# Performance work log

Hardware: AMD Instinct MI355X
Metric: run time of the kernel (lower is better)

Reference implementation:

```python
import jax, jax.numpy as jnp
import numpy as np

NUM_PATCHES = 16
FILTER_SIZE = 4
IN_CHANNELS = 64
OUT_CHANNELS = 256
BATCH = 64


def setup_inputs() -> dict:
    key = jax.random.key(0)
    k1, k2 = jax.random.split(key)
    D = NUM_PATCHES * FILTER_SIZE
    x = jax.random.normal(k1, (BATCH, IN_CHANNELS, D, D), dtype=jnp.float32)
    w = jax.random.normal(
        k2,
        (OUT_CHANNELS, IN_CHANNELS, NUM_PATCHES, NUM_PATCHES, FILTER_SIZE ** 2),
        dtype=jnp.float32,
    )
    return {"x": x, "w": w}


def reference(x, w):
    # x: (N, C, D, D) with D = P*f ; w: (O, C, P, P, f^2)
    N, C, D, _ = x.shape
    O, _, P, _, f2 = w.shape
    f = int(round(f2 ** 0.5))
    # non-overlapping unfold: (N,C,P,f,P,f) -> (N,C,P,P,f,f) -> (N,C,P,P,f^2)
    patches = x.reshape(N, C, P, f, P, f).transpose(0, 1, 2, 4, 3, 5).reshape(N, C, P, P, f2)
    # locally-connected contraction over in_channels and filter elements
    y = jnp.einsum('ncpqf,ocpqf->nopq', patches, w)
    scale = 1.0 / jnp.sqrt(jnp.asarray(f2 * C, dtype=x.dtype))
    return jax.nn.relu(y * scale)
```

## Files before the change

### kernel.cpp

```cpp
#include <hip/hip_runtime.h>


typedef short bf16x8 __attribute__((ext_vector_type(8)));
typedef short bf16x4 __attribute__((ext_vector_type(4)));
typedef float f32x4  __attribute__((ext_vector_type(4)));

__device__ __forceinline__ short f2bf(float f) {
    union { float f; unsigned u; } v; v.f = f;
    return (short)((v.u + 0x7FFFu + ((v.u >> 16) & 1u)) >> 16);
}

__device__ __forceinline__ bf16x8 pack8(f32x4 a, f32x4 b) {
    bf16x8 r;
    r[0] = f2bf(a[0]); r[1] = f2bf(a[1]); r[2] = f2bf(a[2]); r[3] = f2bf(a[3]);
    r[4] = f2bf(b[0]); r[5] = f2bf(b[1]); r[6] = f2bf(b[2]); r[7] = f2bf(b[3]);
    return r;
}

__device__ __forceinline__ void gload16(const void* g, void* l) {
    __builtin_amdgcn_global_load_lds(
        (const __attribute__((address_space(1))) void*)g,
        (__attribute__((address_space(3))) void*)l, 16, 0, 0);
}

__global__ __launch_bounds__(256)
void prep_unfold(const float* __restrict__ x, short* __restrict__ xT) {
    __shared__ __align__(16) char tile[16 * 2056];
    const int bid = blockIdx.x;
    const int p = bid >> 6, c = bid & 63;
    const int t = (int)threadIdx.x;

#pragma unroll
    for (int it = 0; it < 16; ++it) {
        const int id = it * 256 + t;
        const int n = id >> 6, fr = (id >> 4) & 3, cq = id & 15;
        const f32x4 v = *(const f32x4*)(x + (size_t)n * 262144u
                                          + (size_t)c * 4096u
                                          + (size_t)(4 * p + fr) * 64u
                                          + (size_t)(cq * 4));
        bf16x4 b; b[0] = f2bf(v[0]); b[1] = f2bf(v[1]);
                  b[2] = f2bf(v[2]); b[3] = f2bf(v[3]);
        *(bf16x4*)(tile + cq * 2056 + (fr >> 1) * 1024 + n * 16
                        + (fr & 1) * 8) = b;
    }
    __syncthreads();

#pragma unroll
    for (int it = 0; it < 8; ++it) {
        const int id = it * 256 + t;
        const int q = id >> 7, s = id & 127;
        const int koct = s >> 6, n = s & 63;
        const bf16x8 v = *(const bf16x8*)(tile + q * 2056 + koct * 1024 + n * 16);
        *(bf16x8*)(xT + (size_t)(p * 16 + q) * 65536u + (size_t)c * 1024u
                      + (size_t)koct * 512u + (size_t)n * 8u) = v;
    }
}

__global__ __launch_bounds__(512)
void locblock_gemm(const short* __restrict__ xT, const float* __restrict__ w,
                   float* __restrict__ ws2) {
    __shared__ __align__(16) char smem[3][41472];

    const int hw = blockIdx.x;
    const int lb = (hw & 7) * 32 + (hw >> 3);
    const int p  = lb >> 4;
    const int q2 = (lb >> 1) & 7;
    const int oh = lb & 1;

    const int tid  = (int)threadIdx.x;
    const int lane = tid & 63;
    const int wv   = tid >> 6;
    const int l15  = lane & 15;
    const int kq   = lane >> 4;
    const int qw   = wv & 1;
    const int nc   = wv >> 1;

    const int qin  = wv >> 2, acf = (wv >> 1) & 1, akoct = wv & 1;
    const short* asrc = xT + (size_t)(p * 16 + q2 * 2 + qin) * 65536u
                           + (size_t)acf * 1024u + (size_t)akoct * 512u
                           + (size_t)lane * 8u;

    const float* wsrc[4];
#pragma unroll
    for (int j = 0; j < 4; ++j) {
        const int id = j * 512 + tid;
        const int ol = id >> 4, s = id & 15;
        const int u = s ^ (ol & 15);
        wsrc[j] = w + (size_t)(oh * 128 + ol) * 262144u + (size_t)(u >> 3) * 4096u
                    + (size_t)p * 256u + (size_t)(q2 * 32) + (size_t)((u & 7) * 4);
    }

    int aoff[4], boff[2][2];
#pragma unroll
    for (int mf = 0; mf < 4; ++mf)
        aoff[mf] = (qw * 4 + kq) * 1088 + (mf * 16 + l15) * 16;
    {
        const int u1 = (kq >> 1) * 8 + qw * 4 + (kq & 1) * 2;
#pragma unroll
        for (int nf = 0; nf < 2; ++nf) {
            const int ol = nc * 32 + nf * 16 + l15;
            boff[nf][0] = 8704 + ol * 256 + ((u1       ^ l15) * 16);
            boff[nf][1] = 8704 + ol * 256 + (((u1 + 1) ^ l15) * 16);
        }
    }

    f32x4 acc[4][2];
#pragma unroll
    for (int mf = 0; mf < 4; ++mf)
#pragma unroll
        for (int nf = 0; nf < 2; ++nf)
            acc[mf][nf] = (f32x4){0.f, 0.f, 0.f, 0.f};

    auto stage = [&](int t, int buf) {
        char* base = smem[buf];
        gload16(asrc + (size_t)t * 2048u, base + wv * 1088);
#pragma unroll
        for (int j = 0; j < 4; ++j)
            gload16(wsrc[j] + (size_t)t * 8192u,
                    base + 8704 + j * 8192 + wv * 1024);
    };

    auto compute = [&](int buf) {
        const char* Lb = smem[buf];
        bf16x8 av[4], bv[2];
#pragma unroll
        for (int mf = 0; mf < 4; ++mf)
            av[mf] = *(const bf16x8*)(Lb + aoff[mf]);
#pragma unroll
        for (int nf = 0; nf < 2; ++nf)
            bv[nf] = pack8(*(const f32x4*)(Lb + boff[nf][0]),
                           *(const f32x4*)(Lb + boff[nf][1]));
#pragma unroll
        for (int mf = 0; mf < 4; ++mf)
#pragma unroll
            for (int nf = 0; nf < 2; ++nf)
                acc[mf][nf] = __builtin_amdgcn_mfma_f32_16x16x32_bf16(
                    av[mf], bv[nf], acc[mf][nf], 0, 0, 0);
    };

    stage(0, 0);
    stage(1, 1);
    stage(2, 2);
#pragma unroll 1
    for (int t = 0; t < 29; ++t) {
        const int buf = t % 3;
        asm volatile("s_waitcnt vmcnt(10)" ::: "memory");
        __builtin_amdgcn_s_barrier();
        compute(buf);
        asm volatile("s_waitcnt lgkmcnt(0)" ::: "memory");
        __builtin_amdgcn_s_barrier();
        stage(t + 3, buf);
    }
    asm volatile("s_waitcnt vmcnt(10)" ::: "memory");
    __builtin_amdgcn_s_barrier();
    compute(2);
    asm volatile("s_waitcnt vmcnt(5)" ::: "memory");
    __builtin_amdgcn_s_barrier();
    compute(0);
    asm volatile("s_waitcnt vmcnt(0)" ::: "memory");
    __builtin_amdgcn_s_barrier();
    compute(1);

    const float scale = 0.03125f;
    const int pq = p * 16 + q2 * 2 + qw;
#pragma unroll
    for (int mf = 0; mf < 4; ++mf)
#pragma unroll
        for (int nf = 0; nf < 2; ++nf) {
            const int o  = oh * 128 + nc * 32 + nf * 16 + l15;
            const int n0 = mf * 16 + kq * 4;
            f32x4 r;
#pragma unroll
            for (int j = 0; j < 4; ++j)
                r[j] = fmaxf(acc[mf][nf][j] * scale, 0.0f);
            *(f32x4*)(ws2 + (size_t)pq * 16384u + (size_t)o * 64u + n0) = r;
        }
}

__global__ __launch_bounds__(256)
void finish_transpose(const float* __restrict__ ws2, float* __restrict__ out) {
    __shared__ float tile[256 * 68];
    const int o = blockIdx.x;
    const int t = (int)threadIdx.x;

#pragma unroll
    for (int it = 0; it < 16; ++it) {
        const int chunk = it * 256 + t;
        const int pq = chunk >> 4, ng = chunk & 15;
        const f32x4 v = *(const f32x4*)(ws2 + (size_t)pq * 16384u
                                            + (size_t)o * 64u + ng * 4);
        *(f32x4*)&tile[pq * 68 + ng * 4] = v;
    }
    __syncthreads();

    const int n = t >> 2, pqq = t & 3;
#pragma unroll
    for (int i = 0; i < 16; ++i) {
        const int pq0 = i * 16 + pqq * 4;
        f32x4 r;
#pragma unroll
        for (int k = 0; k < 4; ++k)
            r[k] = tile[(pq0 + k) * 68 + n];
        *(f32x4*)(out + (size_t)n * 65536u + (size_t)o * 256u + pq0) = r;
    }
}

extern "C" void kernel_launch(void* const* d_in, const int* in_sizes, int n_in,
                              void* d_out, int out_size, void* d_ws, size_t ws_size,
                              hipStream_t stream) {
    const float* x = (const float*)d_in[0];
    const float* w = (const float*)d_in[1];
    float* out = (float*)d_out;
    short* xT  = (short*)d_ws;
    float* ws2 = (float*)((char*)d_ws + (33554432));
    prep_unfold     <<<dim3(1024), dim3(256), 0, stream>>>(x, xT);
    locblock_gemm   <<<dim3(256),  dim3(512), 0, stream>>>(xT, w, ws2);
    finish_transpose<<<dim3(256),  dim3(256), 0, stream>>>(ws2, out);
}
```

Measured before the change: 104.8 us.

## Replace LDS-direct triple buffering with register-staged double-buffered pipeline

The GEMM kernel no longer uses global_load_lds into a three-stage LDS ring. A operands (bf16 activations) are now loaded straight into registers for each wave's own fragments. Weight tiles are loaded into registers and then written to a two-buffer swizzled LDS area. This cuts LDS footprint and allows the A path to bypass LDS, but it adds register pressure, explicit ds_writes, and a shallower prefetch distance. The hand-placed vmcnt waits must match the new load counts.

```diff
diff --git a/kernel.cpp b/kernel.cpp
--- a/kernel.cpp
+++ b/kernel.cpp
@@ -15,12 +15,6 @@
     r[0] = f2bf(a[0]); r[1] = f2bf(a[1]); r[2] = f2bf(a[2]); r[3] = f2bf(a[3]);
     r[4] = f2bf(b[0]); r[5] = f2bf(b[1]); r[6] = f2bf(b[2]); r[7] = f2bf(b[3]);
     return r;
-}
-
-__device__ __forceinline__ void gload16(const void* g, void* l) {
-    __builtin_amdgcn_global_load_lds(
-        (const __attribute__((address_space(1))) void*)g,
-        (__attribute__((address_space(3))) void*)l, 16, 0, 0);
 }
 
 __global__ __launch_bounds__(256)
@@ -59,7 +53,7 @@
 __global__ __launch_bounds__(512)
 void locblock_gemm(const short* __restrict__ xT, const float* __restrict__ w,
                    float* __restrict__ ws2) {
-    __shared__ __align__(16) char smem[3][41472];
+    __shared__ __align__(16) char smem[2][32768];
 
     const int hw = blockIdx.x;
     const int lb = (hw & 7) * 32 + (hw >> 3);
@@ -75,33 +69,32 @@
     const int qw   = wv & 1;
     const int nc   = wv >> 1;
 
-    const int qin  = wv >> 2, acf = (wv >> 1) & 1, akoct = wv & 1;
-    const short* asrc = xT + (size_t)(p * 16 + q2 * 2 + qin) * 65536u
-                           + (size_t)acf * 1024u + (size_t)akoct * 512u
-                           + (size_t)lane * 8u;
-
-    const float* wsrc[4];
+    const short* asrc = xT + (size_t)(p * 16 + q2 * 2 + qw) * 65536u
+                           + (size_t)(kq >> 1) * 1024u + (size_t)(kq & 1) * 512u
+                           + (size_t)l15 * 8u;
+
+    const float* bsrc[4];
 #pragma unroll
     for (int j = 0; j < 4; ++j) {
         const int id = j * 512 + tid;
-        const int ol = id >> 4, s = id & 15;
-        const int u = s ^ (ol & 15);
-        wsrc[j] = w + (size_t)(oh * 128 + ol) * 262144u + (size_t)(u >> 3) * 4096u
+        const int ol = id >> 4, u = id & 15;
+        bsrc[j] = w + (size_t)(oh * 128 + ol) * 262144u + (size_t)(u >> 3) * 4096u
                     + (size_t)p * 256u + (size_t)(q2 * 32) + (size_t)((u & 7) * 4);
     }
-
-    int aoff[4], boff[2][2];
-#pragma unroll
-    for (int mf = 0; mf < 4; ++mf)
-        aoff[mf] = (qw * 4 + kq) * 1088 + (mf * 16 + l15) * 16;
-    {
-        const int u1 = (kq >> 1) * 8 + qw * 4 + (kq & 1) * 2;
-#pragma unroll
-        for (int nf = 0; nf < 2; ++nf) {
-            const int ol = nc * 32 + nf * 16 + l15;
-            boff[nf][0] = 8704 + ol * 256 + ((u1       ^ l15) * 16);
-            boff[nf][1] = 8704 + ol * 256 + (((u1 + 1) ^ l15) * 16);
-        }
+    int wofs[4];
+#pragma unroll
+    for (int j = 0; j < 4; ++j) {
+        const int id = j * 512 + tid;
+        const int ol = id >> 4;
+        wofs[j] = ol * 64 + (((tid & 15) ^ (ol & 15)) * 4);
+    }
+    const int u1 = (kq >> 1) * 8 + qw * 4 + (kq & 1) * 2;
+    int boff[2][2];
+#pragma unroll
+    for (int nf = 0; nf < 2; ++nf) {
+        const int ol = nc * 32 + nf * 16 + l15;
+        boff[nf][0] = ol * 256 + (((u1)     ^ l15) * 16);
+        boff[nf][1] = ol * 256 + (((u1 + 1) ^ l15) * 16);
     }
 
     f32x4 acc[4][2];
@@ -111,55 +104,67 @@
         for (int nf = 0; nf < 2; ++nf)
             acc[mf][nf] = (f32x4){0.f, 0.f, 0.f, 0.f};
 
-    auto stage = [&](int t, int buf) {
-        char* base = smem[buf];
-        gload16(asrc + (size_t)t * 2048u, base + wv * 1088);
-#pragma unroll
-        for (int j = 0; j < 4; ++j)
-            gload16(wsrc[j] + (size_t)t * 8192u,
-                    base + 8704 + j * 8192 + wv * 1024);
-    };
-
-    auto compute = [&](int buf) {
-        const char* Lb = smem[buf];
-        bf16x8 av[4], bv[2];
-#pragma unroll
-        for (int mf = 0; mf < 4; ++mf)
-            av[mf] = *(const bf16x8*)(Lb + aoff[mf]);
-#pragma unroll
-        for (int nf = 0; nf < 2; ++nf)
-            bv[nf] = pack8(*(const f32x4*)(Lb + boff[nf][0]),
-                           *(const f32x4*)(Lb + boff[nf][1]));
-#pragma unroll
-        for (int mf = 0; mf < 4; ++mf)
-#pragma unroll
-            for (int nf = 0; nf < 2; ++nf)
-                acc[mf][nf] = __builtin_amdgcn_mfma_f32_16x16x32_bf16(
-                    av[mf], bv[nf], acc[mf][nf], 0, 0, 0);
-    };
-
-    stage(0, 0);
-    stage(1, 1);
-    stage(2, 2);
+    bf16x8 as0[4], as1[4];
+    f32x4  bs0[4], bs1[4];
+
+#define ISSUE_A(AS, T)                                                        \
+    _Pragma("unroll") for (int mf = 0; mf < 4; ++mf)                          \
+        AS[mf] = *(const bf16x8*)(asrc + (size_t)(T) * 2048u + mf * 128);
+#define ISSUE_B(BS, T)                                                        \
+    _Pragma("unroll") for (int j = 0; j < 4; ++j)                             \
+        BS[j] = *(const f32x4*)(bsrc[j] + (size_t)(T) * 8192u);
+#define DSWRITE(BS, BUF)                                                      \
+    { float* Wb = (float*)(smem[BUF]);                                        \
+      _Pragma("unroll") for (int j = 0; j < 4; ++j)                           \
+          *(f32x4*)(Wb + wofs[j]) = BS[j]; }
+#define COMPUTE(AS, BUF)                                                      \
+    { const char* Lb = smem[BUF];                                             \
+      bf16x8 bv0 = pack8(*(const f32x4*)(Lb + boff[0][0]),                    \
+                         *(const f32x4*)(Lb + boff[0][1]));                   \
+      bf16x8 bv1 = pack8(*(const f32x4*)(Lb + boff[1][0]),                    \
+                         *(const f32x4*)(Lb + boff[1][1]));                   \
+      _Pragma("unroll") for (int mf = 0; mf < 4; ++mf) {                      \
+          acc[mf][0] = __builtin_amdgcn_mfma_f32_16x16x32_bf16(               \
+              AS[mf], bv0, acc[mf][0], 0, 0, 0);                              \
+          acc[mf][1] = __builtin_amdgcn_mfma_f32_16x16x32_bf16(               \
+              AS[mf], bv1, acc[mf][1], 0, 0, 0);                              \
+      } }
+
+    ISSUE_A(as0, 0); ISSUE_A(as1, 1);
+    ISSUE_B(bs0, 0); ISSUE_B(bs1, 1);
+    asm volatile("s_waitcnt vmcnt(0)" ::: "memory");
+    DSWRITE(bs0, 0);
+    asm volatile("s_waitcnt lgkmcnt(0)" ::: "memory");
+    __builtin_amdgcn_s_barrier();
+
 #pragma unroll 1
-    for (int t = 0; t < 29; ++t) {
-        const int buf = t % 3;
-        asm volatile("s_waitcnt vmcnt(10)" ::: "memory");
-        __builtin_amdgcn_s_barrier();
-        compute(buf);
+    for (int t = 0; t < 30; t += 2) {
+        COMPUTE(as0, 0);
+        ISSUE_A(as0, t + 2);
+        ISSUE_B(bs0, t + 2);
+        asm volatile("s_waitcnt vmcnt(8)" ::: "memory");
+        DSWRITE(bs1, 1);
         asm volatile("s_waitcnt lgkmcnt(0)" ::: "memory");
         __builtin_amdgcn_s_barrier();
-        stage(t + 3, buf);
-    }
-    asm volatile("s_waitcnt vmcnt(10)" ::: "memory");
+        COMPUTE(as1, 1);
+        ISSUE_A(as1, t + 3);
+        ISSUE_B(bs1, t + 3);
+        asm volatile("s_waitcnt vmcnt(8)" ::: "memory");
+        DSWRITE(bs0, 0);
+        asm volatile("s_waitcnt lgkmcnt(0)" ::: "memory");
+        __builtin_amdgcn_s_barrier();
+    }
+    COMPUTE(as0, 0);
+    asm volatile("s_waitcnt vmcnt(0)" ::: "memory");
+    DSWRITE(bs1, 1);
+    asm volatile("s_waitcnt lgkmcnt(0)" ::: "memory");
     __builtin_amdgcn_s_barrier();
-    compute(2);
-    asm volatile("s_waitcnt vmcnt(5)" ::: "memory");
-    __builtin_amdgcn_s_barrier();
-    compute(0);
-    asm volatile("s_waitcnt vmcnt(0)" ::: "memory");
-    __builtin_amdgcn_s_barrier();
-    compute(1);
+    COMPUTE(as1, 1);
+
+#undef ISSUE_A
+#undef ISSUE_B
+#undef DSWRITE
+#undef COMPUTE
 
     const float scale = 0.03125f;
     const int pq = p * 16 + q2 * 2 + qw;
```

Result: no change. 104.4 us (-0.5%).

## Split GEMM output channels into quarters to double block count and occupancy

Applied to the files above, without the earlier changes.

Each GEMM block now covers 64 output channels instead of 128, so the grid grows from 256 to 512 blocks. Per-stage LDS drops from about 41KB to about 25KB, and launch bounds now request 4 blocks per CU. The A tile load is remapped to one 16-byte load per thread, and the wait counts are adjusted to match. The aim is better CU coverage and latency hiding on a bandwidth-bound weight stream. The cost is that each xT tile is loaded twice as often and each block does less work.

```diff
diff --git a/kernel.cpp b/kernel.cpp
--- a/kernel.cpp
+++ b/kernel.cpp
@@ -56,16 +56,18 @@
     }
 }
 
-__global__ __launch_bounds__(512)
+#define A_BYTES 8448
+#define STAGE_BYTES 24832
+__global__ __launch_bounds__(512, 4)
 void locblock_gemm(const short* __restrict__ xT, const float* __restrict__ w,
                    float* __restrict__ ws2) {
-    __shared__ __align__(16) char smem[3][41472];
+    __shared__ __align__(16) char smem[3][STAGE_BYTES];
 
     const int hw = blockIdx.x;
-    const int lb = (hw & 7) * 32 + (hw >> 3);
-    const int p  = lb >> 4;
-    const int q2 = (lb >> 1) & 7;
-    const int oh = lb & 1;
+    const int lb = (hw & 7) * 64 + (hw >> 3);
+    const int p  = lb >> 5;
+    const int q2 = (lb >> 2) & 7;
+    const int oq = lb & 3;
 
     const int tid  = (int)threadIdx.x;
     const int lane = tid & 63;
@@ -75,67 +77,57 @@
     const int qw   = wv & 1;
     const int nc   = wv >> 1;
 
-    const int qin  = wv >> 2, acf = (wv >> 1) & 1, akoct = wv & 1;
-    const short* asrc = xT + (size_t)(p * 16 + q2 * 2 + qin) * 65536u
-                           + (size_t)acf * 1024u + (size_t)akoct * 512u
-                           + (size_t)lane * 8u;
-
-    const float* wsrc[4];
-#pragma unroll
-    for (int j = 0; j < 4; ++j) {
+    const int aqin = tid >> 8, acin = (tid >> 7) & 1;
+    const int akoct = (tid >> 6) & 1, an = tid & 63;
+    const short* asrc = xT + (size_t)(p * 16 + q2 * 2 + aqin) * 65536u
+                           + (size_t)acin * 1024u + (size_t)akoct * 512u
+                           + (size_t)an * 8u;
+    const int adst = aqin * 4224 + acin * 2112 + akoct * 1056 + an * 16;
+
+    const float* bsrc[2];
+#pragma unroll
+    for (int j = 0; j < 2; ++j) {
         const int id = j * 512 + tid;
         const int ol = id >> 4, s = id & 15;
         const int u = s ^ (ol & 15);
-        wsrc[j] = w + (size_t)(oh * 128 + ol) * 262144u + (size_t)(u >> 3) * 4096u
+        bsrc[j] = w + (size_t)(oq * 64 + ol) * 262144u + (size_t)(u >> 3) * 4096u
                     + (size_t)p * 256u + (size_t)(q2 * 32) + (size_t)((u & 7) * 4);
     }
 
-    int aoff[4], boff[2][2];
+    int aoff[4];
 #pragma unroll
     for (int mf = 0; mf < 4; ++mf)
-        aoff[mf] = (qw * 4 + kq) * 1088 + (mf * 16 + l15) * 16;
-    {
-        const int u1 = (kq >> 1) * 8 + qw * 4 + (kq & 1) * 2;
-#pragma unroll
-        for (int nf = 0; nf < 2; ++nf) {
-            const int ol = nc * 32 + nf * 16 + l15;
-            boff[nf][0] = 8704 + ol * 256 + ((u1       ^ l15) * 16);
-            boff[nf][1] = 8704 + ol * 256 + (((u1 + 1) ^ l15) * 16);
-        }
-    }
-
-    f32x4 acc[4][2];
+        aoff[mf] = qw * 4224 + (kq >> 1) * 2112 + (kq & 1) * 1056
+                 + (mf * 16 + l15) * 16;
+    const int u1 = (kq >> 1) * 8 + qw * 4 + (kq & 1) * 2;
+    const int ol0 = nc * 16 + l15;
+    const int boff0 = A_BYTES + ol0 * 256 + ((u1       ^ l15) * 16);
+    const int boff1 = A_BYTES + ol0 * 256 + (((u1 + 1) ^ l15) * 16);
+
+    f32x4 acc[4];
 #pragma unroll
     for (int mf = 0; mf < 4; ++mf)
-#pragma unroll
-        for (int nf = 0; nf < 2; ++nf)
-            acc[mf][nf] = (f32x4){0.f, 0.f, 0.f, 0.f};
+        acc[mf] = (f32x4){0.f, 0.f, 0.f, 0.f};
 
     auto stage = [&](int t, int buf) {
         char* base = smem[buf];
-        gload16(asrc + (size_t)t * 2048u, base + wv * 1088);
-#pragma unroll
-        for (int j = 0; j < 4; ++j)
-            gload16(wsrc[j] + (size_t)t * 8192u,
-                    base + 8704 + j * 8192 + wv * 1024);
+        gload16(asrc + (size_t)t * 2048u, base + adst);
+#pragma unroll
+        for (int j = 0; j < 2; ++j)
+            gload16(bsrc[j] + (size_t)t * 8192u,
+                    base + A_BYTES + j * 8192 + wv * 1024);
     };
 
     auto compute = [&](int buf) {
         const char* Lb = smem[buf];
-        bf16x8 av[4], bv[2];
-#pragma unroll
-        for (int mf = 0; mf < 4; ++mf)
-            av[mf] = *(const bf16x8*)(Lb + aoff[mf]);
-#pragma unroll
-        for (int nf = 0; nf < 2; ++nf)
-            bv[nf] = pack8(*(const f32x4*)(Lb + boff[nf][0]),
-                           *(const f32x4*)(Lb + boff[nf][1]));
-#pragma unroll
-        for (int mf = 0; mf < 4; ++mf)
-#pragma unroll
-            for (int nf = 0; nf < 2; ++nf)
-                acc[mf][nf] = __builtin_amdgcn_mfma_f32_16x16x32_bf16(
-                    av[mf], bv[nf], acc[mf][nf], 0, 0, 0);
+        bf16x8 bv = pack8(*(const f32x4*)(Lb + boff0),
+                          *(const f32x4*)(Lb + boff1));
+#pragma unroll
+        for (int mf = 0; mf < 4; ++mf) {
+            bf16x8 av = *(const bf16x8*)(Lb + aoff[mf]);
+            acc[mf] = __builtin_amdgcn_mfma_f32_16x16x32_bf16(
+                av, bv, acc[mf], 0, 0, 0);
+        }
     };
 
     stage(0, 0);
@@ -144,17 +136,17 @@
 #pragma unroll 1
     for (int t = 0; t < 29; ++t) {
         const int buf = t % 3;
-        asm volatile("s_waitcnt vmcnt(10)" ::: "memory");
+        asm volatile("s_waitcnt vmcnt(6)" ::: "memory");
         __builtin_amdgcn_s_barrier();
         compute(buf);
         asm volatile("s_waitcnt lgkmcnt(0)" ::: "memory");
         __builtin_amdgcn_s_barrier();
         stage(t + 3, buf);
     }
-    asm volatile("s_waitcnt vmcnt(10)" ::: "memory");
+    asm volatile("s_waitcnt vmcnt(6)" ::: "memory");
     __builtin_amdgcn_s_barrier();
     compute(2);
-    asm volatile("s_waitcnt vmcnt(5)" ::: "memory");
+    asm volatile("s_waitcnt vmcnt(3)" ::: "memory");
     __builtin_amdgcn_s_barrier();
     compute(0);
     asm volatile("s_waitcnt vmcnt(0)" ::: "memory");
@@ -163,18 +155,16 @@
 
     const float scale = 0.03125f;
     const int pq = p * 16 + q2 * 2 + qw;
-#pragma unroll
-    for (int mf = 0; mf < 4; ++mf)
-#pragma unroll
-        for (int nf = 0; nf < 2; ++nf) {
-            const int o  = oh * 128 + nc * 32 + nf * 16 + l15;
-            const int n0 = mf * 16 + kq * 4;
-            f32x4 r;
-#pragma unroll
-            for (int j = 0; j < 4; ++j)
-                r[j] = fmaxf(acc[mf][nf][j] * scale, 0.0f);
-            *(f32x4*)(ws2 + (size_t)pq * 16384u + (size_t)o * 64u + n0) = r;
-        }
+    const int o  = oq * 64 + nc * 16 + l15;
+#pragma unroll
+    for (int mf = 0; mf < 4; ++mf) {
+        const int n0 = mf * 16 + kq * 4;
+        f32x4 r;
+#pragma unroll
+        for (int j = 0; j < 4; ++j)
+            r[j] = fmaxf(acc[mf][j] * scale, 0.0f);
+        *(f32x4*)(ws2 + (size_t)pq * 16384u + (size_t)o * 64u + n0) = r;
+    }
 }
 
 __global__ __launch_bounds__(256)
@@ -214,6 +204,6 @@
     short* xT  = (short*)d_ws;
     float* ws2 = (float*)((char*)d_ws + (33554432));
     prep_unfold     <<<dim3(1024), dim3(256), 0, stream>>>(x, xT);
-    locblock_gemm   <<<dim3(256),  dim3(512), 0, stream>>>(xT, w, ws2);
+    locblock_gemm   <<<dim3(512),  dim3(512), 0, stream>>>(xT, w, ws2);
     finish_transpose<<<dim3(256),  dim3(256), 0, stream>>>(ws2, out);
 }
```

Measured after the change: 100.8 us. -3.9%, faster.
